# Optimization experiments

Measured on AMD Instinct MI355X. Metric: run time of the kernel, lower is better.

## Reference

```python
import jax, jax.numpy as jnp
import numpy as np

EMBED_DIM = 2048
HEAD_DIM = 128


def setup_inputs() -> dict:
    key = jax.random.key(0)
    ks = jax.random.split(key, 7)
    B, S = 4, 2048
    lim = 1.0 / np.sqrt(EMBED_DIM)
    hidden_state = jax.random.normal(ks[0], (B, S, EMBED_DIM), dtype=jnp.float32)
    # nn.Linear weights stored as [out, in]; we keep [in, out] for x @ W
    Wq = jax.random.uniform(ks[1], (EMBED_DIM, HEAD_DIM), minval=-lim, maxval=lim, dtype=jnp.float32)
    Wk = jax.random.uniform(ks[2], (EMBED_DIM, HEAD_DIM), minval=-lim, maxval=lim, dtype=jnp.float32)
    Wv = jax.random.uniform(ks[3], (EMBED_DIM, HEAD_DIM), minval=-lim, maxval=lim, dtype=jnp.float32)
    bq = jax.random.uniform(ks[4], (HEAD_DIM,), minval=-lim, maxval=lim, dtype=jnp.float32)
    bk = jax.random.uniform(ks[5], (HEAD_DIM,), minval=-lim, maxval=lim, dtype=jnp.float32)
    bv = jax.random.uniform(ks[6], (HEAD_DIM,), minval=-lim, maxval=lim, dtype=jnp.float32)
    return {"hidden_state": hidden_state, "Wq": Wq, "bq": bq, "Wk": Wk, "bk": bk, "Wv": Wv, "bv": bv}


def reference(hidden_state, Wq, bq, Wk, bk, Wv, bv):
    q = hidden_state @ Wq + bq  # [B,S,D]
    k = hidden_state @ Wk + bk
    v = hidden_state @ Wv + bv
    scale = 1.0 / jnp.sqrt(jnp.asarray(HEAD_DIM, dtype=q.dtype))
    scores = jnp.einsum("bqd,bkd->bqk", q, k) * scale  # [B,S,S]
    S = q.shape[1]
    causal = jnp.triu(jnp.ones((S, S), dtype=bool), k=1)
    scores = jnp.where(causal, jnp.asarray(-1e10, dtype=scores.dtype), scores)
    weights = jax.nn.softmax(scores, axis=-1)
    return jnp.einsum("bqk,bkd->bqd", weights, v)
```

## Files before the change

kernel.cpp:

```cpp
#include <hip/hip_runtime.h>
#include <hip/hip_bf16.h>

#define EMBED 2048
#define SEQ   2048
#define BATCH 4
#define HD    128
#define MROWS (BATCH * SEQ)
#define NTOT  (3 * HD)
#define SCALE 0.08838834764831845f
#define NBQ   (SEQ / 64)
#define NSPL  6
#define FIXM  4.0f

typedef __attribute__((ext_vector_type(8))) short bf16x8;
typedef __attribute__((ext_vector_type(4))) float f32x4;

__device__ __forceinline__ unsigned short f2bf_rne(float x) {
    union { float f; unsigned u; } c; c.f = x;
    unsigned r = c.u + 0x7fffu + ((c.u >> 16) & 1u);
    return (unsigned short)(r >> 16);
}

__device__ __forceinline__ bf16x8 cvt8(f32x4 lo, f32x4 hi) {
    union { unsigned short s[8]; bf16x8 v; } u;
    u.s[0] = f2bf_rne(lo.x); u.s[1] = f2bf_rne(lo.y);
    u.s[2] = f2bf_rne(lo.z); u.s[3] = f2bf_rne(lo.w);
    u.s[4] = f2bf_rne(hi.x); u.s[5] = f2bf_rne(hi.y);
    u.s[6] = f2bf_rne(hi.z); u.s[7] = f2bf_rne(hi.w);
    return u.v;
}

#define MFMA16(a, b, c) __builtin_amdgcn_mfma_f32_16x16x32_bf16((a), (b), (c), 0, 0, 0)

__device__ __forceinline__ void gload_lds16(const void* gp, void* lp) {
    __builtin_amdgcn_global_load_lds(
        (const __attribute__((address_space(1))) void*)gp,
        (__attribute__((address_space(3))) void*)lp, 16, 0, 0);
}

__global__ __launch_bounds__(256) void wt_conv(
    const float* __restrict__ Wq, const float* __restrict__ Wk,
    const float* __restrict__ Wv, unsigned short* __restrict__ WT)
{
    __shared__ float lds[64][129];
    const int tid = threadIdx.x;
    const int blk = blockIdx.x;
    const int mat = blk >> 5;
    const int k0  = (blk & 31) * 64;
    const float* src = (mat == 0) ? Wq : (mat == 1) ? Wk : Wv;

    const float4* s4 = (const float4*)(src + (size_t)k0 * HD);
    for (int i = tid; i < 2048; i += 256) {
        const float4 v = s4[i];
        const int k  = i >> 5;
        const int n4 = (i & 31) * 4;
        lds[k][n4 + 0] = v.x; lds[k][n4 + 1] = v.y;
        lds[k][n4 + 2] = v.z; lds[k][n4 + 3] = v.w;
    }
    __syncthreads();

    const int n  = tid >> 1;
    const int kc = (tid & 1) * 32;
    unsigned short* dst = WT + ((size_t)(mat * HD + n)) * EMBED + k0 + kc;
#pragma unroll
    for (int c = 0; c < 4; ++c) {
        union { unsigned short s[8]; uint4 v; } u;
#pragma unroll
        for (int i = 0; i < 8; ++i)
            u.s[i] = f2bf_rne(lds[kc + c * 8 + i][n]);
        ((uint4*)dst)[c] = u.v;
    }
}

__global__ __launch_bounds__(256, 3) void gemm_qkv(
    const float* __restrict__ H, const unsigned short* __restrict__ WT,
    const float* __restrict__ bq, const float* __restrict__ bk,
    const float* __restrict__ bv,
    unsigned short* __restrict__ Qbf, unsigned short* __restrict__ Kbf,
    unsigned short* __restrict__ VT)
{
    __shared__ float          Abuf[2][64 * 64];
    __shared__ unsigned short Bbuf[2][64 * 64];

    const int tid  = threadIdx.x;
    const int w    = tid >> 6;
    const int lane = tid & 63;
    const int l16  = lane & 15;
    const int quad = lane >> 4;

    const int bid   = blockIdx.x;
    const int xcd   = bid & 7;
    const int local = bid >> 3;
    const int n_blk = local % 6;
    const int m_grp = local / 6;
    const int m0 = (m_grp * 8 + xcd) * 64;
    const int n0 = n_blk * 64;

    const int lr4 = lane >> 4, sl4 = lane & 15;
    const float* agp[4]; int aoff[4];
#pragma unroll
    for (int i = 0; i < 4; ++i) {
        const int r = w * 16 + i * 4 + lr4;
        const int g = sl4 ^ ((i * 4 + lr4) & 15);
        agp[i] = H + (size_t)(m0 + r) * EMBED + g * 4;
        aoff[i] = (w * 16 + i * 4) * 64;
    }
    const int lr8 = lane >> 3, sl8 = lane & 7;
    const unsigned short* bgp[2]; int boff[2];
#pragma unroll
    for (int t = 0; t < 2; ++t) {
        const int r = (w * 2 + t) * 8 + lr8;
        bgp[t] = WT + (size_t)(n0 + r) * EMBED + (sl8 ^ lr8) * 8;
        boff[t] = (w * 2 + t) * 512;
    }

    const int wm = (w >> 1) * 32;
    const int wn = (w & 1) * 32;
    const int xq = l16 & 7;

    f32x4 acc[2][2];
#pragma unroll
    for (int mt = 0; mt < 2; ++mt)
#pragma unroll
        for (int nt = 0; nt < 2; ++nt) {
            f32x4 z = {0.f, 0.f, 0.f, 0.f};
            acc[mt][nt] = z;
        }

#pragma unroll
    for (int i = 0; i < 4; ++i)
        gload_lds16(agp[i], &Abuf[0][aoff[i]]);
#pragma unroll
    for (int t = 0; t < 2; ++t)
        gload_lds16(bgp[t], &Bbuf[0][boff[t]]);
    __syncthreads();

    for (int kt = 0; kt < EMBED / 64; ++kt) {
        const int cur = kt & 1;
        if (kt + 1 < EMBED / 64) {
            const int ko = (kt + 1) * 64;
#pragma unroll
            for (int i = 0; i < 4; ++i)
                gload_lds16(agp[i] + ko, &Abuf[cur ^ 1][aoff[i]]);
#pragma unroll
            for (int t = 0; t < 2; ++t)
                gload_lds16(bgp[t] + ko, &Bbuf[cur ^ 1][boff[t]]);
        }

        bf16x8 aF[2][2], bF[2][2];
#pragma unroll
        for (int mt = 0; mt < 2; ++mt)
#pragma unroll
            for (int ks = 0; ks < 2; ++ks) {
                const float* ab = &Abuf[cur][0] + (wm + mt * 16 + l16) * 64;
                const int c0 = (ks * 4 + quad) * 2;
                const f32x4 lo = *(const f32x4*)(ab + ((c0 ^ l16) * 4));
                const f32x4 hi = *(const f32x4*)(ab + (((c0 + 1) ^ l16) * 4));
                aF[mt][ks] = cvt8(lo, hi);
            }
#pragma unroll
        for (int nt = 0; nt < 2; ++nt)
#pragma unroll
            for (int ks = 0; ks < 2; ++ks)
                bF[nt][ks] = *(const bf16x8*)(
                    &Bbuf[cur][0] + (wn + nt * 16 + l16) * 64 + (((ks * 4 + quad) ^ xq) * 8));
#pragma unroll
        for (int ks = 0; ks < 2; ++ks)
#pragma unroll
            for (int mt = 0; mt < 2; ++mt)
#pragma unroll
                for (int nt = 0; nt < 2; ++nt)
                    acc[mt][nt] = MFMA16(aF[mt][ks], bF[nt][ks], acc[mt][nt]);

        __syncthreads();
    }

#pragma unroll
    for (int nt = 0; nt < 2; ++nt) {
        const int col = n0 + wn + nt * 16 + l16;
        const int sel = col >> 7;
        const int c   = col & (HD - 1);
        const float bias = (sel == 0 ? bq : (sel == 1 ? bk : bv))[c];
#pragma unroll
        for (int mt = 0; mt < 2; ++mt) {
#pragma unroll
            for (int r = 0; r < 4; ++r) {
                const int row = m0 + wm + mt * 16 + quad * 4 + r;
                const float v = acc[mt][nt][r] + bias;
                if (sel == 0) {
                    Qbf[(size_t)row * HD + c] = f2bf_rne(v * SCALE);
                } else if (sel == 1) {
                    Kbf[(size_t)row * HD + c] = f2bf_rne(v);
                } else {
                    const int b = row >> 11;
                    const int s = row & (SEQ - 1);
                    VT[((size_t)b * HD + c) * SEQ + s] = f2bf_rne(v);
                }
            }
        }
    }
}

__global__ __launch_bounds__(256, 3) void flash_attn(
    const unsigned short* __restrict__ Qbf,
    const unsigned short* __restrict__ Kbf,
    const unsigned short* __restrict__ VT,
    float* __restrict__ pO, float* __restrict__ pL)
{
    __shared__ unsigned short Kbuf[64 * 128];
    __shared__ unsigned short Vbuf[128 * 64];
    __shared__ unsigned short plds[4][16 * 72];

    const int tid  = threadIdx.x;
    const int w    = tid >> 6;
    const int lane = tid & 63;
    const int l16  = lane & 15;
    const int quad = lane >> 4;
    const int b    = blockIdx.y;
    const int qb    = NBQ - 1 - blockIdx.x / NSPL;
    const int split = blockIdx.x % NSPL;
    const int q0    = qb * 64;
    const int qw0   = q0 + w * 16;

    bf16x8 aq[4];
    const unsigned short* qrow = Qbf + ((size_t)b * SEQ + qw0 + l16) * HD + quad * 8;
#pragma unroll
    for (int kt = 0; kt < 4; ++kt)
        aq[kt] = *(const bf16x8*)(qrow + kt * 32);

    f32x4 o[8];
#pragma unroll
    for (int nt = 0; nt < 8; ++nt) {
        f32x4 z = {0.f, 0.f, 0.f, 0.f};
        o[nt] = z;
    }
    float l_run[4];
#pragma unroll
    for (int r = 0; r < 4; ++r) l_run[r] = 0.f;

    const int lr4 = lane >> 4, sl4 = lane & 15;
    const int lr8 = lane >> 3, sl8 = lane & 7;
    const unsigned short* kbase = Kbf + (size_t)b * SEQ * HD;
    const unsigned short* vbase = VT + (size_t)b * HD * SEQ;
    unsigned short* myp = &plds[w][0];

    for (int t = split; t <= qb; t += NSPL) {
        const int j0 = t * 64;

#pragma unroll
        for (int i = 0; i < 4; ++i) {
            const int jl = w * 16 + i * 4 + lr4;
            gload_lds16(kbase + (size_t)(j0 + jl) * HD + (sl4 ^ (i * 4 + lr4)) * 8,
                        Kbuf + (w * 16 + i * 4) * 128);
        }
#pragma unroll
        for (int i = 0; i < 4; ++i) {
            const int dr = w * 32 + i * 8 + lr8;
            gload_lds16(vbase + (size_t)dr * SEQ + j0 + (sl8 ^ lr8) * 8,
                        Vbuf + (w * 32 + i * 8) * 64);
        }
        __syncthreads();

        if (j0 <= qw0 + 15) {
            f32x4 s[4];
#pragma unroll
            for (int nt = 0; nt < 4; ++nt) {
                f32x4 z = {0.f, 0.f, 0.f, 0.f};
                s[nt] = z;
            }
#pragma unroll
            for (int kt = 0; kt < 4; ++kt) {
#pragma unroll
                for (int nt = 0; nt < 4; ++nt) {
                    const bf16x8 bk = *(const bf16x8*)(
                        Kbuf + (nt * 16 + l16) * 128 + (((kt * 4 + quad) ^ l16) * 8));
                    s[nt] = MFMA16(aq[kt], bk, s[nt]);
                }
            }

#pragma unroll
            for (int nt = 0; nt < 4; ++nt) {
                const int j = j0 + nt * 16 + l16;
#pragma unroll
                for (int r = 0; r < 4; ++r) {
                    const int q = qw0 + quad * 4 + r;
                    const float sv = (j > q) ? -1e30f : s[nt][r];
                    const float pv = __expf(sv - FIXM);
                    l_run[r] += pv;
                    myp[(quad * 4 + r) * 72 + nt * 16 + l16] = f2bf_rne(pv);
                }
            }
            asm volatile("s_waitcnt lgkmcnt(0)" ::: "memory");
            const bf16x8 pf0 = *(const bf16x8*)(myp + l16 * 72 + quad * 8);
            const bf16x8 pf1 = *(const bf16x8*)(myp + l16 * 72 + 32 + quad * 8);

#pragma unroll
            for (int nt = 0; nt < 8; ++nt) {
                const bf16x8 bv0 = *(const bf16x8*)(
                    Vbuf + (nt * 16 + l16) * 64 + ((quad ^ (l16 & 7)) * 8));
                o[nt] = MFMA16(pf0, bv0, o[nt]);
            }
#pragma unroll
            for (int nt = 0; nt < 8; ++nt) {
                const bf16x8 bv1 = *(const bf16x8*)(
                    Vbuf + (nt * 16 + l16) * 64 + (((4 + quad) ^ (l16 & 7)) * 8));
                o[nt] = MFMA16(pf1, bv1, o[nt]);
            }
        }
        __syncthreads();
    }

#pragma unroll
    for (int r = 0; r < 4; ++r) {
#pragma unroll
        for (int d = 1; d < 16; d <<= 1)
            l_run[r] += __shfl_xor(l_run[r], d);
    }
    const int part = (b * NBQ + qb) * NSPL + split;
    float* po = pO + (size_t)part * (64 * HD);
#pragma unroll
    for (int nt = 0; nt < 8; ++nt)
#pragma unroll
        for (int r = 0; r < 4; ++r)
            po[(w * 16 + quad * 4 + r) * HD + nt * 16 + l16] = o[nt][r];
    if (l16 == 0) {
#pragma unroll
        for (int r = 0; r < 4; ++r)
            pL[part * 64 + w * 16 + quad * 4 + r] = l_run[r];
    }
}

__global__ __launch_bounds__(256) void attn_merge(
    const float* __restrict__ pO, const float* __restrict__ pL,
    float* __restrict__ out)
{
    const int bx  = blockIdx.x;
    const int b   = blockIdx.y;
    const int qb  = bx >> 3;
    const int tid = threadIdx.x;
    const int r   = (bx & 7) * 8 + (tid >> 5);
    const int d0  = (tid & 31) * 4;
    const int p0  = (b * NBQ + qb) * NSPL;

    float L = 0.f;
#pragma unroll
    for (int s = 0; s < NSPL; ++s) L += pL[(p0 + s) * 64 + r];
    const float invL = 1.0f / L;

    float4 acc = {0.f, 0.f, 0.f, 0.f};
#pragma unroll
    for (int s = 0; s < NSPL; ++s) {
        const float4 v = *(const float4*)(
            pO + (size_t)(p0 + s) * (64 * HD) + r * HD + d0);
        acc.x += v.x; acc.y += v.y; acc.z += v.z; acc.w += v.w;
    }
    float* op = out + ((size_t)b * SEQ + qb * 64 + r) * HD + d0;
    op[0] = acc.x * invL;
    op[1] = acc.y * invL;
    op[2] = acc.z * invL;
    op[3] = acc.w * invL;
}

extern "C" void kernel_launch(void* const* d_in, const int* in_sizes, int n_in,
                              void* d_out, int out_size, void* d_ws, size_t ws_size,
                              hipStream_t stream)
{
    const float* h  = (const float*)d_in[0];
    const float* Wq = (const float*)d_in[1];
    const float* bq = (const float*)d_in[2];
    const float* Wk = (const float*)d_in[3];
    const float* bk = (const float*)d_in[4];
    const float* Wv = (const float*)d_in[5];
    const float* bv = (const float*)d_in[6];
    float* out = (float*)d_out;

    float* pO = (float*)d_ws;
    float* pL = pO + (size_t)BATCH * NBQ * NSPL * 64 * HD;
    unsigned short* Qbf = (unsigned short*)(pL + (size_t)BATCH * NBQ * NSPL * 64);
    unsigned short* Kbf = Qbf + (size_t)MROWS * HD;
    unsigned short* VT  = Kbf + (size_t)MROWS * HD;
    unsigned short* WT  = VT  + (size_t)MROWS * HD;

    wt_conv<<<96, 256, 0, stream>>>(Wq, Wk, Wv, WT);
    gemm_qkv<<<768, 256, 0, stream>>>(h, WT, bq, bk, bv, Qbf, Kbf, VT);
    flash_attn<<<dim3(NBQ * NSPL, BATCH), 256, 0, stream>>>(Qbf, Kbf, VT, pO, pL);
    attn_merge<<<dim3(NBQ * 8, BATCH), 256, 0, stream>>>(pO, pL, out);
}
```

Measured before the change: 163.8 us.

## Deepen QKV GEMM pipeline to four stages with 32-wide K tiles

Replaces the double-buffered 64-wide K loop in the QKV projection GEMM with a four-stage ring of 32-wide K tiles. Loads run three tiles ahead, and explicit vmcnt waits plus barriers replace the per-iteration __syncthreads. The swizzles are adjusted for the narrower rows. The aim is to hide global load latency better at the same LDS footprint, at the cost of more barriers per unit of work and hand-counted vmcnt values that must match the issued loads exactly.

After: 180.0 us. 9.9% more time.

```diff
diff --git a/kernel.cpp b/kernel.cpp
--- a/kernel.cpp
+++ b/kernel.cpp
@@ -79,8 +79,8 @@
     unsigned short* __restrict__ Qbf, unsigned short* __restrict__ Kbf,
     unsigned short* __restrict__ VT)
 {
-    __shared__ float          Abuf[2][64 * 64];
-    __shared__ unsigned short Bbuf[2][64 * 64];
+    __shared__ float          Abuf[4][64 * 32];
+    __shared__ unsigned short Bbuf[4][64 * 32];
 
     const int tid  = threadIdx.x;
     const int w    = tid >> 6;
@@ -96,27 +96,23 @@
     const int m0 = (m_grp * 8 + xcd) * 64;
     const int n0 = n_blk * 64;
 
-    const int lr4 = lane >> 4, sl4 = lane & 15;
-    const float* agp[4]; int aoff[4];
-#pragma unroll
-    for (int i = 0; i < 4; ++i) {
-        const int r = w * 16 + i * 4 + lr4;
-        const int g = sl4 ^ ((i * 4 + lr4) & 15);
+    const float* agp[2]; int aoff[2];
+#pragma unroll
+    for (int i = 0; i < 2; ++i) {
+        const int r = w * 16 + i * 8 + (lane >> 3);
+        const int g = (lane & 7) ^ (lane >> 3);
         agp[i] = H + (size_t)(m0 + r) * EMBED + g * 4;
-        aoff[i] = (w * 16 + i * 4) * 64;
-    }
-    const int lr8 = lane >> 3, sl8 = lane & 7;
-    const unsigned short* bgp[2]; int boff[2];
-#pragma unroll
-    for (int t = 0; t < 2; ++t) {
-        const int r = (w * 2 + t) * 8 + lr8;
-        bgp[t] = WT + (size_t)(n0 + r) * EMBED + (sl8 ^ lr8) * 8;
-        boff[t] = (w * 2 + t) * 512;
-    }
+        aoff[i] = (w * 16 + i * 8) * 32;
+    }
+    const unsigned short* bgp =
+        WT + (size_t)(n0 + w * 16 + (lane >> 2)) * EMBED
+           + (((lane & 3) ^ ((lane >> 3) & 3)) * 8);
+    const int boff = w * 512;
 
     const int wm = (w >> 1) * 32;
     const int wn = (w & 1) * 32;
-    const int xq = l16 & 7;
+    const int x7 = l16 & 7;
+    const int x3 = (l16 >> 1) & 3;
 
     f32x4 acc[2][2];
 #pragma unroll
@@ -127,53 +123,61 @@
             acc[mt][nt] = z;
         }
 
-#pragma unroll
-    for (int i = 0; i < 4; ++i)
-        gload_lds16(agp[i], &Abuf[0][aoff[i]]);
-#pragma unroll
-    for (int t = 0; t < 2; ++t)
-        gload_lds16(bgp[t], &Bbuf[0][boff[t]]);
-    __syncthreads();
-
-    for (int kt = 0; kt < EMBED / 64; ++kt) {
-        const int cur = kt & 1;
-        if (kt + 1 < EMBED / 64) {
-            const int ko = (kt + 1) * 64;
-#pragma unroll
-            for (int i = 0; i < 4; ++i)
-                gload_lds16(agp[i] + ko, &Abuf[cur ^ 1][aoff[i]]);
-#pragma unroll
-            for (int t = 0; t < 2; ++t)
-                gload_lds16(bgp[t] + ko, &Bbuf[cur ^ 1][boff[t]]);
-        }
-
-        bf16x8 aF[2][2], bF[2][2];
-#pragma unroll
-        for (int mt = 0; mt < 2; ++mt)
-#pragma unroll
-            for (int ks = 0; ks < 2; ++ks) {
-                const float* ab = &Abuf[cur][0] + (wm + mt * 16 + l16) * 64;
-                const int c0 = (ks * 4 + quad) * 2;
-                const f32x4 lo = *(const f32x4*)(ab + ((c0 ^ l16) * 4));
-                const f32x4 hi = *(const f32x4*)(ab + (((c0 + 1) ^ l16) * 4));
-                aF[mt][ks] = cvt8(lo, hi);
-            }
-#pragma unroll
-        for (int nt = 0; nt < 2; ++nt)
-#pragma unroll
-            for (int ks = 0; ks < 2; ++ks)
-                bF[nt][ks] = *(const bf16x8*)(
-                    &Bbuf[cur][0] + (wn + nt * 16 + l16) * 64 + (((ks * 4 + quad) ^ xq) * 8));
-#pragma unroll
-        for (int ks = 0; ks < 2; ++ks)
-#pragma unroll
-            for (int mt = 0; mt < 2; ++mt)
-#pragma unroll
-                for (int nt = 0; nt < 2; ++nt)
-                    acc[mt][nt] = MFMA16(aF[mt][ks], bF[nt][ks], acc[mt][nt]);
-
-        __syncthreads();
-    }
+#define STAGE(bufi, kk) do {                                              \
+        gload_lds16(agp[0] + (size_t)(kk) * 32, &Abuf[(bufi)][aoff[0]]);  \
+        gload_lds16(agp[1] + (size_t)(kk) * 32, &Abuf[(bufi)][aoff[1]]);  \
+        gload_lds16(bgp    + (size_t)(kk) * 32, &Bbuf[(bufi)][boff]);     \
+    } while (0)
+
+#define COMPUTE(bufi) do {                                                \
+        bf16x8 aF[2], bF[2];                                              \
+        _Pragma("unroll")                                                 \
+        for (int mt = 0; mt < 2; ++mt) {                                  \
+            const float* ab = &Abuf[(bufi)][(wm + mt * 16 + l16) * 32];   \
+            const f32x4 lo = *(const f32x4*)(ab + (((2 * quad)     ^ x7) * 4)); \
+            const f32x4 hi = *(const f32x4*)(ab + (((2 * quad + 1) ^ x7) * 4)); \
+            aF[mt] = cvt8(lo, hi);                                        \
+        }                                                                 \
+        _Pragma("unroll")                                                 \
+        for (int nt = 0; nt < 2; ++nt)                                    \
+            bF[nt] = *(const bf16x8*)(                                    \
+                &Bbuf[(bufi)][(wn + nt * 16 + l16) * 32 + ((quad ^ x3) * 8)]); \
+        _Pragma("unroll")                                                 \
+        for (int mt = 0; mt < 2; ++mt)                                    \
+            _Pragma("unroll")                                             \
+            for (int nt = 0; nt < 2; ++nt)                                \
+                acc[mt][nt] = MFMA16(aF[mt], bF[nt], acc[mt][nt]);        \
+    } while (0)
+
+#define WAITBAR(n) do {                                                   \
+        asm volatile("s_waitcnt vmcnt(" #n ")" ::: "memory");             \
+        __builtin_amdgcn_s_barrier();                                     \
+        __builtin_amdgcn_sched_barrier(0);                                \
+    } while (0)
+
+    STAGE(0, 0);
+    STAGE(1, 1);
+    STAGE(2, 2);
+
+#pragma unroll 4
+    for (int kt = 0; kt < 60; ++kt) {
+        WAITBAR(6);
+        STAGE((kt + 3) & 3, kt + 3);
+        COMPUTE(kt & 3);
+    }
+    WAITBAR(6);
+    STAGE(3, 63);
+    COMPUTE(0);
+    WAITBAR(6);
+    COMPUTE(1);
+    WAITBAR(3);
+    COMPUTE(2);
+    WAITBAR(0);
+    COMPUTE(3);
+
+#undef STAGE
+#undef COMPUTE
+#undef WAITBAR
 
 #pragma unroll
     for (int nt = 0; nt < 2; ++nt) {
```
